# Optimization experiments

Measured on AMD Instinct MI355X. Metric: run time of the kernel, lower is better.

## Reference

```python
import jax, jax.numpy as jnp
import numpy as np

N = 50000      # nodes
E = 800000     # edges
IN = 128       # in_channels
HID = 64       # hidden_channels (per head)
HEADS = 2      # GAT heads
OUT = 64       # out_channels (classes)


def segment_softmax(e, seg, num_segments):
    # softmax of per-edge scores grouped by destination node
    m = jax.ops.segment_max(e, seg, num_segments=num_segments)
    ex = jnp.exp(e - m[seg])
    s = jax.ops.segment_sum(ex, seg, num_segments=num_segments)
    return ex / s[seg]


def setup_inputs() -> dict:
    key = jax.random.key(0)
    ks = jax.random.split(key, 12)
    sc = 0.05
    return {
        "x": jax.random.normal(ks[0], (N, IN), dtype=jnp.float32),
        "edge_index": jax.random.randint(ks[1], (2, E), 0, N),
        # GATConv params: lin (no bias), att_src/att_dst, output bias
        "W1": jax.random.normal(ks[2], (IN, HEADS * HID), dtype=jnp.float32) * sc,
        "att_src": jax.random.normal(ks[3], (HEADS, HID), dtype=jnp.float32) * sc,
        "att_dst": jax.random.normal(ks[4], (HEADS, HID), dtype=jnp.float32) * sc,
        "b1": jnp.zeros((HEADS * HID,), dtype=jnp.float32),
        # TransformerConv params (heads=1): q/k/v linears + skip linear
        "Wq": jax.random.normal(ks[5], (HEADS * HID, OUT), dtype=jnp.float32) * sc,
        "bq": jnp.zeros((OUT,), dtype=jnp.float32),
        "Wk": jax.random.normal(ks[6], (HEADS * HID, OUT), dtype=jnp.float32) * sc,
        "bk": jnp.zeros((OUT,), dtype=jnp.float32),
        "Wv": jax.random.normal(ks[7], (HEADS * HID, OUT), dtype=jnp.float32) * sc,
        "bv": jnp.zeros((OUT,), dtype=jnp.float32),
        "Wskip": jax.random.normal(ks[8], (HEADS * HID, OUT), dtype=jnp.float32) * sc,
        "bskip": jnp.zeros((OUT,), dtype=jnp.float32),
    }


def reference(x, edge_index, W1, att_src, att_dst, b1,
              Wq, bq, Wk, bk, Wv, bv, Wskip, bskip):
    n = x.shape[0]
    # ---- GATConv (concat=True, add_self_loops=True, negative_slope=0.2) ----
    loops = jnp.arange(n)
    src = jnp.concatenate([edge_index[0], loops])  # message source j
    dst = jnp.concatenate([edge_index[1], loops])  # message target i
    h = (x @ W1).reshape(n, HEADS, HID)            # [N,H,C]
    a_src = (h * att_src).sum(-1)                  # [N,H]
    a_dst = (h * att_dst).sum(-1)                  # [N,H]
    e = jax.nn.leaky_relu(a_src[src] + a_dst[dst], 0.2)   # [E+N,H]
    alpha = segment_softmax(e, dst, n)                     # [E+N,H]
    out1 = jax.ops.segment_sum(alpha[..., None] * h[src], dst, num_segments=n)
    x1 = jax.nn.relu(out1.reshape(n, HEADS * HID) + b1)    # [N,H*C]
    # ---- TransformerConv (heads=1, root_weight=True, no self-loops) ----
    q = x1 @ Wq + bq
    k = x1 @ Wk + bk
    v = x1 @ Wv + bv
    s2, d2 = edge_index[0], edge_index[1]
    scores = (q[d2] * k[s2]).sum(-1) / jnp.sqrt(jnp.float32(OUT))  # [E]
    al = segment_softmax(scores, d2, n)
    agg = jax.ops.segment_sum(al[:, None] * v[s2], d2, num_segments=n)
    out = agg + x1 @ Wskip + bskip
    return jax.nn.log_softmax(out, axis=1)
```

## Files before the change

### kernel.cpp

```cpp
#include <hip/hip_runtime.h>
#include <math.h>

typedef unsigned short u16;
typedef unsigned int u32;
typedef unsigned char u8;

using bf16x8 = __attribute__((ext_vector_type(8))) short;
using f32x4  = __attribute__((ext_vector_type(4))) float;
typedef __attribute__((ext_vector_type(2))) float vf2;

__device__ __forceinline__ float lrelu02(float x){ return x > 0.f ? x : 0.2f * x; }

__device__ __forceinline__ float bf2f(u16 u){
  union { u32 i; float f; } v; v.i = ((u32)u) << 16; return v.f;
}
__device__ __forceinline__ u16 f2bf(float f){
  union { float ff; u32 i; } v; v.ff = f;
  u32 x = v.i;
  return (u16)((x + 0x7fffu + ((x >> 16) & 1u)) >> 16);
}
__device__ __forceinline__ u32 pack2(float lo, float hi){
  return (u32)f2bf(lo) | ((u32)f2bf(hi) << 16);
}
__device__ __forceinline__ void unpack8(uint4 w, float* f){
  f[0] = bf2f((u16)(w.x & 0xffffu)); f[1] = bf2f((u16)(w.x >> 16));
  f[2] = bf2f((u16)(w.y & 0xffffu)); f[3] = bf2f((u16)(w.y >> 16));
  f[4] = bf2f((u16)(w.z & 0xffffu)); f[5] = bf2f((u16)(w.z >> 16));
  f[6] = bf2f((u16)(w.w & 0xffffu)); f[7] = bf2f((u16)(w.w >> 16));
}
__device__ __forceinline__ u8 f2fp8(float v){
  return (u8)(__builtin_amdgcn_cvt_pk_fp8_f32(v, v, 0, false) & 0xff);
}

__global__ __launch_bounds__(256) void cast_x_kernel(const float* __restrict__ x,
                                                     u16* __restrict__ xbf, int total8){
  int i = blockIdx.x * 256 + threadIdx.x;
  if (i >= total8) return;
  const float4* x4 = (const float4*)x;
  float4 a = x4[(size_t)i * 2];
  float4 b = x4[(size_t)i * 2 + 1];
  uint4 w;
  w.x = pack2(a.x, a.y);
  w.y = pack2(a.z, a.w);
  w.z = pack2(b.x, b.y);
  w.w = pack2(b.z, b.w);
  ((uint4*)xbf)[i] = w;
}

__global__ __launch_bounds__(256) void prep_w_kernel(const float* __restrict__ W1,
                                                     const float* __restrict__ Wq,
                                                     const float* __restrict__ Wk,
                                                     const float* __restrict__ Wv,
                                                     const float* __restrict__ Ws,
                                                     const float* __restrict__ att_src,
                                                     const float* __restrict__ att_dst,
                                                     u16* __restrict__ w1t,
                                                     u16* __restrict__ wt2,
                                                     u16* __restrict__ wxt){
  int idx = blockIdx.x * 256 + threadIdx.x;
  if (idx < 16384){
    int j = idx >> 7, k = idx & 127;
    w1t[j * 128 + k] = f2bf(W1[k * 128 + j]);
  } else if (idx < 49152){
    int i = idx - 16384;
    int mat = i >> 13;
    int r = i & 8191;
    int j = r >> 7, k = r & 127;
    const float* W = (mat == 0) ? Wq : (mat == 1) ? Wk : (mat == 2) ? Wv : Ws;
    wt2[(mat * 64 + j) * 128 + k] = f2bf(W[k * 64 + j]);
  } else if (idx < 49664){
    int i = idx - 49152;
    int j = i >> 7, k = i & 127;
    const float* av = (j & 2) ? att_dst : att_src;
    int head = j & 1;
    float s = 0.f;
#pragma unroll 8
    for (int c = 0; c < 64; c++) s += W1[k * 128 + head * 64 + c] * av[head * 64 + c];
    wxt[j * 128 + k] = f2bf(s);
  } else if (idx < 51200){
    int i = idx - 49664;
    wxt[512 + i] = 0;
  }
}

__global__ __launch_bounds__(256) void gemm1_mfma(const u16* __restrict__ xbf,
                                                  const u16* __restrict__ w1t,
                                                  const u16* __restrict__ wxt,
                                                  u16* __restrict__ h2,
                                                  float* __restrict__ asrc,
                                                  float* __restrict__ adst, int n){
  int wid = threadIdx.x >> 6, lane = threadIdx.x & 63;
  int rl = lane & 15, kh = lane >> 4;
  int br = blockIdx.x * 64 + wid * 16;
  int arow = br + rl; if (arow > n - 1) arow = n - 1;
  const u16* abase = xbf + (size_t)arow * 128 + kh * 8;
  f32x4 acc[9];
#pragma unroll
  for (int t = 0; t < 9; t++) acc[t] = (f32x4){0.f, 0.f, 0.f, 0.f};
#pragma unroll
  for (int ks = 0; ks < 4; ks++){
    bf16x8 a = *(const bf16x8*)(abase + ks * 32);
#pragma unroll
    for (int t = 0; t < 8; t++){
      bf16x8 b = *(const bf16x8*)(w1t + (size_t)(t * 16 + rl) * 128 + ks * 32 + kh * 8);
      acc[t] = __builtin_amdgcn_mfma_f32_16x16x32_bf16(a, b, acc[t], 0, 0, 0);
    }
    bf16x8 bx = *(const bf16x8*)(wxt + (size_t)rl * 128 + ks * 32 + kh * 8);
    acc[8] = __builtin_amdgcn_mfma_f32_16x16x32_bf16(a, bx, acc[8], 0, 0, 0);
  }
  int orow0 = br + kh * 4;
#pragma unroll
  for (int r = 0; r < 4; r++){
    int orow = orow0 + r;
    if (orow < n){
      u16* hp = h2 + (size_t)orow * 128 + rl;
#pragma unroll
      for (int t = 0; t < 8; t++) hp[t * 16] = f2bf(acc[t][r]);
      if (rl < 4){
        float vlv = acc[8][r];
        if (rl < 2) asrc[orow * 2 + rl] = vlv;
        else        adst[orow * 2 + (rl - 2)] = vlv;
      }
    }
  }
}

__global__ __launch_bounds__(256) void gemm2_mfma(const u16* __restrict__ x1bf,
                                                  const u16* __restrict__ wt2,
                                                  const float* __restrict__ bq,
                                                  const float* __restrict__ bk,
                                                  const float* __restrict__ bv,
                                                  const float* __restrict__ bs,
                                                  float* __restrict__ q,
                                                  u8* __restrict__ kv8,
                                                  float* __restrict__ skip, int n){
  int wid = threadIdx.x >> 6, lane = threadIdx.x & 63;
  int rl = lane & 15, kh = lane >> 4;
  int br = blockIdx.x * 64 + wid * 16;
  int arow = br + rl; if (arow > n - 1) arow = n - 1;
  const u16* abase = x1bf + (size_t)arow * 128 + kh * 8;
  f32x4 acc[16];
#pragma unroll
  for (int t = 0; t < 16; t++) acc[t] = (f32x4){0.f, 0.f, 0.f, 0.f};
#pragma unroll
  for (int ks = 0; ks < 4; ks++){
    bf16x8 a = *(const bf16x8*)(abase + ks * 32);
#pragma unroll
    for (int t = 0; t < 16; t++){
      bf16x8 b = *(const bf16x8*)(wt2 + (size_t)(t * 16 + rl) * 128 + ks * 32 + kh * 8);
      acc[t] = __builtin_amdgcn_mfma_f32_16x16x32_bf16(a, b, acc[t], 0, 0, 0);
    }
  }
  float bias_t[16];
#pragma unroll
  for (int t = 0; t < 16; t++){
    const float* bb = (t < 4) ? bq : (t < 8) ? bk : (t < 12) ? bv : bs;
    bias_t[t] = bb[(t & 3) * 16 + rl];
  }
  int orow0 = br + kh * 4;
#pragma unroll
  for (int r = 0; r < 4; r++){
    int orow = orow0 + r;
    if (orow >= n) continue;
#pragma unroll
    for (int t = 0; t < 16; t++){
      int c = (t & 3) * 16 + rl;
      float val = acc[t][r] + bias_t[t];
      if (t < 4)       q[(size_t)orow * 64 + c]    = val;
      else if (t < 8)  kv8[(size_t)orow * 128 + (c >> 3) * 16 + (c & 7)]     = f2fp8(val);
      else if (t < 12) kv8[(size_t)orow * 128 + (c >> 3) * 16 + 8 + (c & 7)] = f2fp8(val);
      else             skip[(size_t)orow * 64 + c] = val;
    }
  }
}

__global__ __launch_bounds__(256) void bucket_hist_kernel(const int* __restrict__ dst,
                                                          int* __restrict__ bc, int E){
  __shared__ int h[512];
  for (int i = threadIdx.x; i < 512; i += 256) h[i] = 0;
  __syncthreads();
  int base = blockIdx.x * 4096;
#pragma unroll
  for (int i = 0; i < 16; i++){
    int e = base + i * 256 + threadIdx.x;
    if (e < E) atomicAdd(&h[dst[e] >> 7], 1);
  }
  __syncthreads();
  for (int i = threadIdx.x; i < 512; i += 256)
    if (h[i]) atomicAdd(&bc[i], h[i]);
}

__global__ __launch_bounds__(256) void bucket_scan_kernel(const int* __restrict__ bc,
                                                          int* __restrict__ bbase,
                                                          int* __restrict__ bcur){
  __shared__ int tmp[5];
  int tid = threadIdx.x;
  int c0 = bc[2 * tid], c1 = bc[2 * tid + 1];
  int s = c0 + c1, incl = s;
  int lane = tid & 63, wid = tid >> 6;
#pragma unroll
  for (int o = 1; o < 64; o <<= 1){
    int t = __shfl_up(incl, o);
    if (lane >= o) incl += t;
  }
  if (lane == 63) tmp[wid] = incl;
  __syncthreads();
  if (tid == 0){
    int run = 0;
#pragma unroll
    for (int w2 = 0; w2 < 4; w2++){ int t = tmp[w2]; tmp[w2] = run; run += t; }
    tmp[4] = run;
  }
  __syncthreads();
  int excl = tmp[wid] + incl - s;
  bbase[2 * tid]     = excl;      bbase[2 * tid + 1] = excl + c0;
  bcur[2 * tid]      = excl;      bcur[2 * tid + 1]  = excl + c0;
  if (tid == 255) bbase[512] = tmp[4];
}

__global__ __launch_bounds__(256) void multisplit_kernel(const int* __restrict__ src,
                                                         const int* __restrict__ dst,
                                                         int* __restrict__ bcur,
                                                         uint2* __restrict__ ebuf, int E){
  __shared__ int h[512];
  __shared__ int gb[512];
  __shared__ int cur[512];
  int tid = threadIdx.x;
  for (int i = tid; i < 512; i += 256){ h[i] = 0; cur[i] = 0; }
  __syncthreads();
  int base = blockIdx.x * 4096;
  int myd[16];
#pragma unroll
  for (int i = 0; i < 16; i++){
    int e = base + i * 256 + tid;
    myd[i] = (e < E) ? dst[e] : -1;
    if (myd[i] >= 0) atomicAdd(&h[myd[i] >> 7], 1);
  }
  __syncthreads();
  for (int i = tid; i < 512; i += 256){
    int c = h[i];
    gb[i] = c ? atomicAdd(&bcur[i], c) : 0;
  }
  __syncthreads();
#pragma unroll
  for (int i = 0; i < 16; i++){
    if (myd[i] >= 0){
      int e = base + i * 256 + tid;
      int b = myd[i] >> 7;
      int r = atomicAdd(&cur[b], 1);
      uint2 ed; ed.x = (u32)src[e]; ed.y = (u32)myd[i];
      ebuf[gb[b] + r] = ed;
    }
  }
}

__global__ __launch_bounds__(256) void bucket_csr_kernel(const uint2* __restrict__ ebuf,
                                                         const int* __restrict__ bbase,
                                                         int* __restrict__ offsets,
                                                         int* __restrict__ csr,
                                                         int n, int E, int nb){
  __shared__ int deg[128];
  __shared__ int loff[128];
  __shared__ int cur[128];
  int b = blockIdx.x, tid = threadIdx.x;
  int base = bbase[b], end = bbase[b + 1];
  if (tid < 128) deg[tid] = 0;
  __syncthreads();
  for (int e = base + tid; e < end; e += 256)
    atomicAdd(&deg[ebuf[e].y & 127], 1);
  __syncthreads();
  if (tid < 64){
    int v0 = deg[2 * tid], v1 = deg[2 * tid + 1];
    int s = v0 + v1, incl = s;
#pragma unroll
    for (int o = 1; o < 64; o <<= 1){
      int t = __shfl_up(incl, o);
      if (tid >= o) incl += t;
    }
    int excl = incl - s;
    loff[2 * tid] = excl; loff[2 * tid + 1] = excl + v0;
  }
  __syncthreads();
  int node0 = b << 7;
  if (tid < 128){
    cur[tid] = loff[tid];
    int node = node0 + tid;
    if (node < n) offsets[node] = base + loff[tid];
  }
  if (b == nb - 1 && tid == 0) offsets[n] = E;
  __syncthreads();
  for (int e = base + tid; e < end; e += 256){
    uint2 ed = ebuf[e];
    int r = atomicAdd(&cur[ed.y & 127], 1);
    csr[base + r] = (int)ed.x;
  }
}

__global__ __launch_bounds__(256) void gat_agg_kernel(const u16* __restrict__ h2,
                                                      const float* __restrict__ asrc,
                                                      const float* __restrict__ adst,
                                                      const int* __restrict__ off,
                                                      const int* __restrict__ csr_src,
                                                      const float* __restrict__ b1,
                                                      u16* __restrict__ x1bf, int n){
  int node = blockIdx.x * 4 + (threadIdx.x >> 6);
  int lane = threadIdx.x & 63;
  if (node >= n) return;
  int s0 = off[node];
  int d  = off[node + 1] - s0;
  int g = lane >> 3;
  int sub = lane & 7;
  int chb = sub * 16;
  int head = sub >> 2;
  float2 ad  = ((const float2*)adst)[node];
  float2 asl = ((const float2*)asrc)[node];
  float ad_own = head ? ad.y : ad.x;
  float pself = __expf(lrelu02((head ? asl.y : asl.x) + ad_own));
  float acc[16];
#pragma unroll
  for (int i = 0; i < 16; i++) acc[i] = 0.f;
  float ps = 0.f;
#pragma unroll 2
  for (int base = 0; base < d; base += 8){
    int idx = base + g;
    bool valid = idx < d;
    int sj = csr_src[s0 + (valid ? idx : d - 1)];
    float2 as = ((const float2*)asrc)[sj];
    float p = valid ? __expf(lrelu02((head ? as.y : as.x) + ad_own)) : 0.f;
    ps += p;
    const u16* hr = h2 + (size_t)sj * 128 + chb;
    uint4 ha = *(const uint4*)hr;
    uint4 hb = *(const uint4*)(hr + 8);
    float f[16];
    unpack8(ha, f); unpack8(hb, f + 8);
#pragma unroll
    for (int i = 0; i < 16; i++) acc[i] = fmaf(p, f[i], acc[i]);
  }
#pragma unroll
  for (int o = 8; o <= 32; o <<= 1){
#pragma unroll
    for (int i = 0; i < 16; i++) acc[i] += __shfl_xor(acc[i], o);
    ps += __shfl_xor(ps, o);
  }
  if (lane < 8){
    float st = ps + pself;
    const u16* hs = h2 + (size_t)node * 128 + chb;
    uint4 ha = *(const uint4*)hs;
    uint4 hb = *(const uint4*)(hs + 8);
    float f[16];
    unpack8(ha, f); unpack8(hb, f + 8);
    const float4* bp = (const float4*)(b1 + chb);
    float4 bv0 = bp[0], bv1 = bp[1], bv2 = bp[2], bv3 = bp[3];
    float bb[16] = {bv0.x, bv0.y, bv0.z, bv0.w, bv1.x, bv1.y, bv1.z, bv1.w,
                    bv2.x, bv2.y, bv2.z, bv2.w, bv3.x, bv3.y, bv3.z, bv3.w};
    float inv = 1.f / st;
    u32 wv[8];
#pragma unroll
    for (int i = 0; i < 8; i++){
      float v0 = fmaxf(fmaf(pself, f[2*i],   acc[2*i])   * inv + bb[2*i],   0.f);
      float v1 = fmaxf(fmaf(pself, f[2*i+1], acc[2*i+1]) * inv + bb[2*i+1], 0.f);
      wv[i] = pack2(v0, v1);
    }
    uint4 o0 = {wv[0], wv[1], wv[2], wv[3]};
    uint4 o1 = {wv[4], wv[5], wv[6], wv[7]};
    u16* xp = x1bf + (size_t)node * 128 + chb;
    *(uint4*)xp = o0;
    *(uint4*)(xp + 8) = o1;
  }
}

__global__ __launch_bounds__(256) void trans_agg_kernel(const float* __restrict__ q,
                                                        const u8* __restrict__ kv8,
                                                        const float* __restrict__ skip,
                                                        const int* __restrict__ off,
                                                        const int* __restrict__ csr_src,
                                                        float* __restrict__ out, int n){
  int node = blockIdx.x * 4 + (threadIdx.x >> 6);
  int lane = threadIdx.x & 63;
  if (node >= n) return;
  int s0 = off[node];
  int d  = off[node + 1] - s0;
  int g = lane >> 3;
  int sub = lane & 7;
  const float4* qp = (const float4*)(q + (size_t)node * 64 + sub * 8);
  float4 qa = qp[0], qb = qp[1];
  float acc[8];
#pragma unroll
  for (int i = 0; i < 8; i++) acc[i] = 0.f;
  float ps = 0.f;
#pragma unroll 2
  for (int base = 0; base < d; base += 8){
    int idx = base + g;
    bool valid = idx < d;
    int sj = csr_src[s0 + (valid ? idx : d - 1)];
    uint4 w = *(const uint4*)(kv8 + (size_t)sj * 128 + sub * 16);
    vf2 k0 = __builtin_amdgcn_cvt_pk_f32_fp8((int)w.x, false);
    vf2 k1 = __builtin_amdgcn_cvt_pk_f32_fp8((int)w.x, true);
    vf2 k2 = __builtin_amdgcn_cvt_pk_f32_fp8((int)w.y, false);
    vf2 k3 = __builtin_amdgcn_cvt_pk_f32_fp8((int)w.y, true);
    float part = qa.x * k0[0];
    part = fmaf(qa.y, k0[1], part);
    part = fmaf(qa.z, k1[0], part);
    part = fmaf(qa.w, k1[1], part);
    part = fmaf(qb.x, k2[0], part);
    part = fmaf(qb.y, k2[1], part);
    part = fmaf(qb.z, k3[0], part);
    part = fmaf(qb.w, k3[1], part);
    part += __shfl_xor(part, 1);
    part += __shfl_xor(part, 2);
    part += __shfl_xor(part, 4);
    float p = valid ? __expf(part * 0.125f) : 0.f;
    ps += p;
    vf2 v0 = __builtin_amdgcn_cvt_pk_f32_fp8((int)w.z, false);
    vf2 v1 = __builtin_amdgcn_cvt_pk_f32_fp8((int)w.z, true);
    vf2 v2 = __builtin_amdgcn_cvt_pk_f32_fp8((int)w.w, false);
    vf2 v3 = __builtin_amdgcn_cvt_pk_f32_fp8((int)w.w, true);
    acc[0] = fmaf(p, v0[0], acc[0]);
    acc[1] = fmaf(p, v0[1], acc[1]);
    acc[2] = fmaf(p, v1[0], acc[2]);
    acc[3] = fmaf(p, v1[1], acc[3]);
    acc[4] = fmaf(p, v2[0], acc[4]);
    acc[5] = fmaf(p, v2[1], acc[5]);
    acc[6] = fmaf(p, v3[0], acc[6]);
    acc[7] = fmaf(p, v3[1], acc[7]);
  }
#pragma unroll
  for (int o = 8; o <= 32; o <<= 1){
#pragma unroll
    for (int i = 0; i < 8; i++) acc[i] += __shfl_xor(acc[i], o);
    ps += __shfl_xor(ps, o);
  }
  if (lane < 8){
    const float4* sp = (const float4*)(skip + (size_t)node * 64 + sub * 8);
    float4 s0v = sp[0], s1v = sp[1];
    float sk[8] = {s0v.x, s0v.y, s0v.z, s0v.w, s1v.x, s1v.y, s1v.z, s1v.w};
    float inv = (d > 0) ? 1.f / ps : 0.f;
    float val[8];
    float mx = -3.0e38f;
#pragma unroll
    for (int i = 0; i < 8; i++){ val[i] = sk[i] + acc[i] * inv; mx = fmaxf(mx, val[i]); }
    mx = fmaxf(mx, __shfl_xor(mx, 1));
    mx = fmaxf(mx, __shfl_xor(mx, 2));
    mx = fmaxf(mx, __shfl_xor(mx, 4));
    float se = 0.f;
#pragma unroll
    for (int i = 0; i < 8; i++){ val[i] -= mx; se += __expf(val[i]); }
    se += __shfl_xor(se, 1);
    se += __shfl_xor(se, 2);
    se += __shfl_xor(se, 4);
    float lse = __logf(se);
    float* op = out + (size_t)node * 64 + sub * 8;
    float4 o0 = {val[0] - lse, val[1] - lse, val[2] - lse, val[3] - lse};
    float4 o4 = {val[4] - lse, val[5] - lse, val[6] - lse, val[7] - lse};
    *(float4*)(op)     = o0;
    *(float4*)(op + 4) = o4;
  }
}

extern "C" void kernel_launch(void* const* d_in, const int* in_sizes, int n_in,
                              void* d_out, int out_size, void* d_ws, size_t ws_size,
                              hipStream_t stream) {
  const float* x       = (const float*)d_in[0];
  const int*   ei      = (const int*)d_in[1];
  const float* W1      = (const float*)d_in[2];
  const float* att_src = (const float*)d_in[3];
  const float* att_dst = (const float*)d_in[4];
  const float* b1      = (const float*)d_in[5];
  const float* Wq = (const float*)d_in[6];  const float* bq = (const float*)d_in[7];
  const float* Wk = (const float*)d_in[8];  const float* bk = (const float*)d_in[9];
  const float* Wv = (const float*)d_in[10]; const float* bv = (const float*)d_in[11];
  const float* Ws = (const float*)d_in[12]; const float* bs = (const float*)d_in[13];
  float* out = (float*)d_out;

  int n = in_sizes[0] / 128;
  int E = in_sizes[1] / 2;
  const int* src = ei;
  const int* dst = ei + E;
  int nb = (n + 127) >> 7;

  char* w = (char*)d_ws;
  auto alloc = [&](size_t bytes) -> void* {
    void* p = (void*)w;
    w += (bytes + 255) & ~(size_t)255;
    return p;
  };
  u16*  xbf  = (u16*)alloc((size_t)n * 128 * 2);
  u16*  h2   = (u16*)alloc((size_t)n * 128 * 2);
  float* asrc = (float*)alloc((size_t)n * 2 * 4);
  float* adst = (float*)alloc((size_t)n * 2 * 4);
  u16*  x1bf = (u16*)alloc((size_t)n * 128 * 2);
  float* qq   = (float*)alloc((size_t)n * 64 * 4);
  u8*   kv8  = (u8*)alloc((size_t)n * 128);
  float* skip = (float*)alloc((size_t)n * 64 * 4);
  int* offsets = (int*)alloc((size_t)(n + 1) * 4);
  int* csr     = (int*)alloc((size_t)E * 4);
  int* bc      = (int*)alloc(516 * 4);
  int* bbase   = (int*)alloc(516 * 4);
  int* bcur    = (int*)alloc(516 * 4);
  u16*  w1t  = (u16*)alloc((size_t)128 * 128 * 2);
  u16*  wt2  = (u16*)alloc((size_t)256 * 128 * 2);
  u16*  wxt  = (u16*)alloc((size_t)16 * 128 * 2);
  uint2* ebuf = (uint2*)xbf;

  int eblocks = (E + 4095) / 4096;

  hipMemsetAsync(bc, 0, 513 * 4, stream);
  cast_x_kernel<<<(n * 16 + 255) / 256, 256, 0, stream>>>(x, xbf, n * 16);
  prep_w_kernel<<<200, 256, 0, stream>>>(W1, Wq, Wk, Wv, Ws, att_src, att_dst,
                                         w1t, wt2, wxt);
  gemm1_mfma<<<(n + 63) / 64, 256, 0, stream>>>(xbf, w1t, wxt, h2, asrc, adst, n);

  bucket_hist_kernel<<<eblocks, 256, 0, stream>>>(dst, bc, E);
  bucket_scan_kernel<<<1, 256, 0, stream>>>(bc, bbase, bcur);
  multisplit_kernel<<<eblocks, 256, 0, stream>>>(src, dst, bcur, ebuf, E);
  bucket_csr_kernel<<<nb, 256, 0, stream>>>(ebuf, bbase, offsets, csr, n, E, nb);

  gat_agg_kernel<<<(n + 3) / 4, 256, 0, stream>>>(h2, asrc, adst, offsets, csr, b1, x1bf, n);

  gemm2_mfma<<<(n + 63) / 64, 256, 0, stream>>>(x1bf, wt2, bq, bk, bv, bs,
                                                qq, kv8, skip, n);
  trans_agg_kernel<<<(n + 3) / 4, 256, 0, stream>>>(qq, kv8, skip, offsets, csr,
                                                    out, n);
}
```

Measured before the change: 186.5 us.

## Gather GAT features as fp8 and use packed float2 FMAs in aggregations

```diff
diff --git a/kernel.cpp b/kernel.cpp
--- a/kernel.cpp
+++ b/kernel.cpp
@@ -22,14 +22,11 @@
 __device__ __forceinline__ u32 pack2(float lo, float hi){
   return (u32)f2bf(lo) | ((u32)f2bf(hi) << 16);
 }
-__device__ __forceinline__ void unpack8(uint4 w, float* f){
-  f[0] = bf2f((u16)(w.x & 0xffffu)); f[1] = bf2f((u16)(w.x >> 16));
-  f[2] = bf2f((u16)(w.y & 0xffffu)); f[3] = bf2f((u16)(w.y >> 16));
-  f[4] = bf2f((u16)(w.z & 0xffffu)); f[5] = bf2f((u16)(w.z >> 16));
-  f[6] = bf2f((u16)(w.w & 0xffffu)); f[7] = bf2f((u16)(w.w >> 16));
-}
 __device__ __forceinline__ u8 f2fp8(float v){
   return (u8)(__builtin_amdgcn_cvt_pk_fp8_f32(v, v, 0, false) & 0xff);
+}
+__device__ __forceinline__ vf2 fma2(vf2 a, vf2 b, vf2 c){
+  return __builtin_elementwise_fma(a, b, c);
 }
 
 __global__ __launch_bounds__(256) void cast_x_kernel(const float* __restrict__ x,
@@ -45,6 +42,25 @@
   w.z = pack2(b.x, b.y);
   w.w = pack2(b.z, b.w);
   ((uint4*)xbf)[i] = w;
+}
+
+__global__ __launch_bounds__(256) void cast_h_kernel(const u16* __restrict__ h2,
+                                                     u8* __restrict__ h8, int total16){
+  int i = blockIdx.x * 256 + threadIdx.x;
+  if (i >= total16) return;
+  const uint4* hp = (const uint4*)(h2 + (size_t)i * 16);
+  uint4 a = hp[0], b = hp[1];
+  u32 w0 = 0, w1 = 0, w2 = 0, w3 = 0;
+  w0 = __builtin_amdgcn_cvt_pk_fp8_f32(bf2f((u16)(a.x & 0xffffu)), bf2f((u16)(a.x >> 16)), w0, false);
+  w0 = __builtin_amdgcn_cvt_pk_fp8_f32(bf2f((u16)(a.y & 0xffffu)), bf2f((u16)(a.y >> 16)), w0, true);
+  w1 = __builtin_amdgcn_cvt_pk_fp8_f32(bf2f((u16)(a.z & 0xffffu)), bf2f((u16)(a.z >> 16)), w1, false);
+  w1 = __builtin_amdgcn_cvt_pk_fp8_f32(bf2f((u16)(a.w & 0xffffu)), bf2f((u16)(a.w >> 16)), w1, true);
+  w2 = __builtin_amdgcn_cvt_pk_fp8_f32(bf2f((u16)(b.x & 0xffffu)), bf2f((u16)(b.x >> 16)), w2, false);
+  w2 = __builtin_amdgcn_cvt_pk_fp8_f32(bf2f((u16)(b.y & 0xffffu)), bf2f((u16)(b.y >> 16)), w2, true);
+  w3 = __builtin_amdgcn_cvt_pk_fp8_f32(bf2f((u16)(b.z & 0xffffu)), bf2f((u16)(b.z >> 16)), w3, false);
+  w3 = __builtin_amdgcn_cvt_pk_fp8_f32(bf2f((u16)(b.w & 0xffffu)), bf2f((u16)(b.w >> 16)), w3, true);
+  uint4 o = {w0, w1, w2, w3};
+  ((uint4*)h8)[i] = o;
 }
 
 __global__ __launch_bounds__(256) void prep_w_kernel(const float* __restrict__ W1,
@@ -296,7 +312,7 @@
   }
 }
 
-__global__ __launch_bounds__(256) void gat_agg_kernel(const u16* __restrict__ h2,
+__global__ __launch_bounds__(256) void gat_agg_kernel(const u8* __restrict__ h8,
                                                       const float* __restrict__ asrc,
                                                       const float* __restrict__ adst,
                                                       const int* __restrict__ off,
@@ -316,9 +332,9 @@
   float2 asl = ((const float2*)asrc)[node];
   float ad_own = head ? ad.y : ad.x;
   float pself = __expf(lrelu02((head ? asl.y : asl.x) + ad_own));
-  float acc[16];
-#pragma unroll
-  for (int i = 0; i < 16; i++) acc[i] = 0.f;
+  vf2 acc[8];
+#pragma unroll
+  for (int i = 0; i < 8; i++) acc[i] = (vf2){0.f, 0.f};
   float ps = 0.f;
 #pragma unroll 2
   for (int base = 0; base < d; base += 8){
@@ -328,27 +344,38 @@
     float2 as = ((const float2*)asrc)[sj];
     float p = valid ? __expf(lrelu02((head ? as.y : as.x) + ad_own)) : 0.f;
     ps += p;
-    const u16* hr = h2 + (size_t)sj * 128 + chb;
-    uint4 ha = *(const uint4*)hr;
-    uint4 hb = *(const uint4*)(hr + 8);
-    float f[16];
-    unpack8(ha, f); unpack8(hb, f + 8);
-#pragma unroll
-    for (int i = 0; i < 16; i++) acc[i] = fmaf(p, f[i], acc[i]);
+    uint4 w = *(const uint4*)(h8 + (size_t)sj * 128 + chb);
+    vf2 p2 = {p, p};
+    acc[0] = fma2(p2, __builtin_amdgcn_cvt_pk_f32_fp8((int)w.x, false), acc[0]);
+    acc[1] = fma2(p2, __builtin_amdgcn_cvt_pk_f32_fp8((int)w.x, true),  acc[1]);
+    acc[2] = fma2(p2, __builtin_amdgcn_cvt_pk_f32_fp8((int)w.y, false), acc[2]);
+    acc[3] = fma2(p2, __builtin_amdgcn_cvt_pk_f32_fp8((int)w.y, true),  acc[3]);
+    acc[4] = fma2(p2, __builtin_amdgcn_cvt_pk_f32_fp8((int)w.z, false), acc[4]);
+    acc[5] = fma2(p2, __builtin_amdgcn_cvt_pk_f32_fp8((int)w.z, true),  acc[5]);
+    acc[6] = fma2(p2, __builtin_amdgcn_cvt_pk_f32_fp8((int)w.w, false), acc[6]);
+    acc[7] = fma2(p2, __builtin_amdgcn_cvt_pk_f32_fp8((int)w.w, true),  acc[7]);
   }
 #pragma unroll
   for (int o = 8; o <= 32; o <<= 1){
 #pragma unroll
-    for (int i = 0; i < 16; i++) acc[i] += __shfl_xor(acc[i], o);
+    for (int i = 0; i < 8; i++){
+      acc[i][0] += __shfl_xor(acc[i][0], o);
+      acc[i][1] += __shfl_xor(acc[i][1], o);
+    }
     ps += __shfl_xor(ps, o);
   }
   if (lane < 8){
     float st = ps + pself;
-    const u16* hs = h2 + (size_t)node * 128 + chb;
-    uint4 ha = *(const uint4*)hs;
-    uint4 hb = *(const uint4*)(hs + 8);
-    float f[16];
-    unpack8(ha, f); unpack8(hb, f + 8);
+    uint4 w = *(const uint4*)(h8 + (size_t)node * 128 + chb);
+    vf2 pf2 = {pself, pself};
+    acc[0] = fma2(pf2, __builtin_amdgcn_cvt_pk_f32_fp8((int)w.x, false), acc[0]);
+    acc[1] = fma2(pf2, __builtin_amdgcn_cvt_pk_f32_fp8((int)w.x, true),  acc[1]);
+    acc[2] = fma2(pf2, __builtin_amdgcn_cvt_pk_f32_fp8((int)w.y, false), acc[2]);
+    acc[3] = fma2(pf2, __builtin_amdgcn_cvt_pk_f32_fp8((int)w.y, true),  acc[3]);
+    acc[4] = fma2(pf2, __builtin_amdgcn_cvt_pk_f32_fp8((int)w.z, false), acc[4]);
+    acc[5] = fma2(pf2, __builtin_amdgcn_cvt_pk_f32_fp8((int)w.z, true),  acc[5]);
+    acc[6] = fma2(pf2, __builtin_amdgcn_cvt_pk_f32_fp8((int)w.w, false), acc[6]);
+    acc[7] = fma2(pf2, __builtin_amdgcn_cvt_pk_f32_fp8((int)w.w, true),  acc[7]);
     const float4* bp = (const float4*)(b1 + chb);
     float4 bv0 = bp[0], bv1 = bp[1], bv2 = bp[2], bv3 = bp[3];
     float bb[16] = {bv0.x, bv0.y, bv0.z, bv0.w, bv1.x, bv1.y, bv1.z, bv1.w,
@@ -357,8 +384,8 @@
     u32 wv[8];
 #pragma unroll
     for (int i = 0; i < 8; i++){
-      float v0 = fmaxf(fmaf(pself, f[2*i],   acc[2*i])   * inv + bb[2*i],   0.f);
-      float v1 = fmaxf(fmaf(pself, f[2*i+1], acc[2*i+1]) * inv + bb[2*i+1], 0.f);
+      float v0 = fmaxf(acc[i][0] * inv + bb[2*i],   0.f);
+      float v1 = fmaxf(acc[i][1] * inv + bb[2*i+1], 0.f);
       wv[i] = pack2(v0, v1);
     }
     uint4 o0 = {wv[0], wv[1], wv[2], wv[3]};
@@ -382,11 +409,11 @@
   int d  = off[node + 1] - s0;
   int g = lane >> 3;
   int sub = lane & 7;
-  const float4* qp = (const float4*)(q + (size_t)node * 64 + sub * 8);
-  float4 qa = qp[0], qb = qp[1];
-  float acc[8];
-#pragma unroll
-  for (int i = 0; i < 8; i++) acc[i] = 0.f;
+  const vf2* qp = (const vf2*)(q + (size_t)node * 64 + sub * 8);
+  vf2 q0 = qp[0], q1 = qp[1], q2 = qp[2], q3 = qp[3];
+  vf2 acc[4];
+#pragma unroll
+  for (int i = 0; i < 4; i++) acc[i] = (vf2){0.f, 0.f};
   float ps = 0.f;
 #pragma unroll 2
   for (int base = 0; base < d; base += 8){
@@ -394,40 +421,30 @@
     bool valid = idx < d;
     int sj = csr_src[s0 + (valid ? idx : d - 1)];
     uint4 w = *(const uint4*)(kv8 + (size_t)sj * 128 + sub * 16);
-    vf2 k0 = __builtin_amdgcn_cvt_pk_f32_fp8((int)w.x, false);
-    vf2 k1 = __builtin_amdgcn_cvt_pk_f32_fp8((int)w.x, true);
-    vf2 k2 = __builtin_amdgcn_cvt_pk_f32_fp8((int)w.y, false);
-    vf2 k3 = __builtin_amdgcn_cvt_pk_f32_fp8((int)w.y, true);
-    float part = qa.x * k0[0];
-    part = fmaf(qa.y, k0[1], part);
-    part = fmaf(qa.z, k1[0], part);
-    part = fmaf(qa.w, k1[1], part);
-    part = fmaf(qb.x, k2[0], part);
-    part = fmaf(qb.y, k2[1], part);
-    part = fmaf(qb.z, k3[0], part);
-    part = fmaf(qb.w, k3[1], part);
+    vf2 d2 = {0.f, 0.f};
+    d2 = fma2(q0, __builtin_amdgcn_cvt_pk_f32_fp8((int)w.x, false), d2);
+    d2 = fma2(q1, __builtin_amdgcn_cvt_pk_f32_fp8((int)w.x, true),  d2);
+    d2 = fma2(q2, __builtin_amdgcn_cvt_pk_f32_fp8((int)w.y, false), d2);
+    d2 = fma2(q3, __builtin_amdgcn_cvt_pk_f32_fp8((int)w.y, true),  d2);
+    float part = d2[0] + d2[1];
     part += __shfl_xor(part, 1);
     part += __shfl_xor(part, 2);
     part += __shfl_xor(part, 4);
     float p = valid ? __expf(part * 0.125f) : 0.f;
     ps += p;
-    vf2 v0 = __builtin_amdgcn_cvt_pk_f32_fp8((int)w.z, false);
-    vf2 v1 = __builtin_amdgcn_cvt_pk_f32_fp8((int)w.z, true);
-    vf2 v2 = __builtin_amdgcn_cvt_pk_f32_fp8((int)w.w, false);
-    vf2 v3 = __builtin_amdgcn_cvt_pk_f32_fp8((int)w.w, true);
-    acc[0] = fmaf(p, v0[0], acc[0]);
-    acc[1] = fmaf(p, v0[1], acc[1]);
-    acc[2] = fmaf(p, v1[0], acc[2]);
-    acc[3] = fmaf(p, v1[1], acc[3]);
-    acc[4] = fmaf(p, v2[0], acc[4]);
-    acc[5] = fmaf(p, v2[1], acc[5]);
-    acc[6] = fmaf(p, v3[0], acc[6]);
-    acc[7] = fmaf(p, v3[1], acc[7]);
+    vf2 p2 = {p, p};
+    acc[0] = fma2(p2, __builtin_amdgcn_cvt_pk_f32_fp8((int)w.z, false), acc[0]);
+    acc[1] = fma2(p2, __builtin_amdgcn_cvt_pk_f32_fp8((int)w.z, true),  acc[1]);
+    acc[2] = fma2(p2, __builtin_amdgcn_cvt_pk_f32_fp8((int)w.w, false), acc[2]);
+    acc[3] = fma2(p2, __builtin_amdgcn_cvt_pk_f32_fp8((int)w.w, true),  acc[3]);
   }
 #pragma unroll
   for (int o = 8; o <= 32; o <<= 1){
 #pragma unroll
-    for (int i = 0; i < 8; i++) acc[i] += __shfl_xor(acc[i], o);
+    for (int i = 0; i < 4; i++){
+      acc[i][0] += __shfl_xor(acc[i][0], o);
+      acc[i][1] += __shfl_xor(acc[i][1], o);
+    }
     ps += __shfl_xor(ps, o);
   }
   if (lane < 8){
@@ -438,7 +455,10 @@
     float val[8];
     float mx = -3.0e38f;
 #pragma unroll
-    for (int i = 0; i < 8; i++){ val[i] = sk[i] + acc[i] * inv; mx = fmaxf(mx, val[i]); }
+    for (int i = 0; i < 8; i++){
+      val[i] = sk[i] + acc[i >> 1][i & 1] * inv;
+      mx = fmaxf(mx, val[i]);
+    }
     mx = fmaxf(mx, __shfl_xor(mx, 1));
     mx = fmaxf(mx, __shfl_xor(mx, 2));
     mx = fmaxf(mx, __shfl_xor(mx, 4));
@@ -486,6 +506,7 @@
   };
   u16*  xbf  = (u16*)alloc((size_t)n * 128 * 2);
   u16*  h2   = (u16*)alloc((size_t)n * 128 * 2);
+  u8*   h8   = (u8*)alloc((size_t)n * 128);
   float* asrc = (float*)alloc((size_t)n * 2 * 4);
   float* adst = (float*)alloc((size_t)n * 2 * 4);
   u16*  x1bf = (u16*)alloc((size_t)n * 128 * 2);
@@ -509,13 +530,14 @@
   prep_w_kernel<<<200, 256, 0, stream>>>(W1, Wq, Wk, Wv, Ws, att_src, att_dst,
                                          w1t, wt2, wxt);
   gemm1_mfma<<<(n + 63) / 64, 256, 0, stream>>>(xbf, w1t, wxt, h2, asrc, adst, n);
+  cast_h_kernel<<<(n * 8 + 255) / 256, 256, 0, stream>>>(h2, h8, n * 8);
 
   bucket_hist_kernel<<<eblocks, 256, 0, stream>>>(dst, bc, E);
   bucket_scan_kernel<<<1, 256, 0, stream>>>(bc, bbase, bcur);
   multisplit_kernel<<<eblocks, 256, 0, stream>>>(src, dst, bcur, ebuf, E);
   bucket_csr_kernel<<<nb, 256, 0, stream>>>(ebuf, bbase, offsets, csr, n, E, nb);
 
-  gat_agg_kernel<<<(n + 3) / 4, 256, 0, stream>>>(h2, asrc, adst, offsets, csr, b1, x1bf, n);
+  gat_agg_kernel<<<(n + 3) / 4, 256, 0, stream>>>(h8, asrc, adst, offsets, csr, b1, x1bf, n);
 
   gemm2_mfma<<<(n + 63) / 64, 256, 0, stream>>>(x1bf, wt2, bq, bk, bv, bs,
                                                 qq, kv8, skip, n);
```

Result: no change. 187.3 us (+0.4%).
